# Kernel optimization log

Hardware: AMD Instinct MI355X
Metric: run time of the kernel (lower is better)

The kernel has to match this reference:

```python
import jax, jax.numpy as jnp
import numpy as np

B, S, H = 2, 2048, 1024
NUM_HEAD = 16
HEAD_HIDDEN = H // NUM_HEAD
SCALE = float(np.sqrt(HEAD_HIDDEN))  # 8.0
INF = 10000000000.0


def setup_inputs() -> dict:
    key = jax.random.key(0)
    ks = jax.random.split(key, 12)
    std = 1.0 / np.sqrt(H)
    mk = lambda k: (jax.random.normal(k, (H, H), jnp.float32) * std)
    return {
        "query": jax.random.normal(ks[0], (B, S, H), jnp.float32),
        "key": jax.random.normal(ks[1], (B, S, H), jnp.float32),
        "value": jax.random.normal(ks[2], (B, S, H), jnp.float32),
        "att_mask": jnp.ones((B, 1, 1, S), jnp.float32),
        "wq": mk(ks[3]), "bq": jnp.zeros((H,), jnp.float32),
        "wk": mk(ks[4]), "bk": jnp.zeros((H,), jnp.float32),
        "wv": mk(ks[5]), "bv": jnp.zeros((H,), jnp.float32),
        "wo": mk(ks[6]), "bo": jnp.zeros((H,), jnp.float32),
    }


def reference(query, key, value, att_mask, wq, bq, wk, bk, wv, bv, wo, bo):
    # projections (weights stored as [in, out])
    q = query @ wq + bq
    k = key @ wk + bk
    v = value @ wv + bv
    # split heads: [B, S, nH, hd]
    q = q.reshape(B, S, NUM_HEAD, HEAD_HIDDEN)
    k = k.reshape(B, S, NUM_HEAD, HEAD_HIDDEN)
    v = v.reshape(B, S, NUM_HEAD, HEAD_HIDDEN)
    # scores [B, nH, Sq, Sk], first divide by scale
    att = jnp.einsum("bqhd,bkhd->bhqk", q, k) / SCALE
    # additive mask applied BEFORE the second scale division (faithful quirk)
    att = att + (1.0 - att_mask) * (-INF)
    att = jax.nn.softmax(att / SCALE, axis=-1)
    out = jnp.einsum("bhqk,bkhd->bqhd", att, v).reshape(B, S, H)
    return out @ wo + bo
```

## Files before the change

kernel.cpp:

```cpp
#include <hip/hip_runtime.h>
#include <cstdint>

typedef unsigned short u16;
typedef __attribute__((ext_vector_type(8))) short bf16x8;
typedef __attribute__((ext_vector_type(4))) float f32x4;

#define S_LEN 2048
#define HDIM  1024
#define NHEAD 16

__device__ __forceinline__ float bf2f(u16 u){ return __uint_as_float(((uint32_t)u) << 16); }
__device__ __forceinline__ u16 f2bf(float f){
  uint32_t x = __float_as_uint(f);
  return (u16)((x + 0x7fffu + ((x >> 16) & 1u)) >> 16);
}

__device__ __forceinline__ void gload_lds16(const void* g, void* l){
  __builtin_amdgcn_global_load_lds((const __attribute__((address_space(1))) void*)g,
                                   (__attribute__((address_space(3))) void*)l, 16, 0, 0);
}

__global__ __launch_bounds__(256) void k_cvt3(const float* __restrict__ q, const float* __restrict__ k,
                                              const float* __restrict__ v, u16* __restrict__ oq,
                                              u16* __restrict__ ok, u16* __restrict__ ov){
  int z = blockIdx.y;
  const float* in = z == 0 ? q : (z == 1 ? k : v);
  u16* out = z == 0 ? oq : (z == 1 ? ok : ov);
  int i = blockIdx.x * 256 + threadIdx.x;
  float4 f0 = *(const float4*)&in[(size_t)i * 8];
  float4 f1 = *(const float4*)&in[(size_t)i * 8 + 4];
  bf16x8 o;
  o[0] = (short)f2bf(f0.x); o[1] = (short)f2bf(f0.y);
  o[2] = (short)f2bf(f0.z); o[3] = (short)f2bf(f0.w);
  o[4] = (short)f2bf(f1.x); o[5] = (short)f2bf(f1.y);
  o[6] = (short)f2bf(f1.z); o[7] = (short)f2bf(f1.w);
  *(bf16x8*)&out[(size_t)i * 8] = o;
}

__global__ __launch_bounds__(256) void k_tr_w4(const float* __restrict__ w0, const float* __restrict__ w1,
                                               const float* __restrict__ w2, const float* __restrict__ w3,
                                               u16* __restrict__ o0, u16* __restrict__ o1,
                                               u16* __restrict__ o2, u16* __restrict__ o3){
  int z = blockIdx.z;
  const float* in = z == 0 ? w0 : (z == 1 ? w1 : (z == 2 ? w2 : w3));
  u16* out = z == 0 ? o0 : (z == 1 ? o1 : (z == 2 ? o2 : o3));
  __shared__ float t[64][65];
  int r0 = threadIdx.x >> 6;
  int c  = threadIdx.x & 63;
  int bx = blockIdx.x * 64, by = blockIdx.y * 64;
  #pragma unroll
  for (int i = 0; i < 64; i += 4) t[r0 + i][c] = in[(size_t)(by + r0 + i) * 1024 + bx + c];
  __syncthreads();
  #pragma unroll
  for (int i = 0; i < 64; i += 4) out[(size_t)(bx + r0 + i) * 1024 + by + c] = f2bf(t[c][r0 + i]);
}

__global__ __launch_bounds__(256) void k_gemm_qkv(const u16* __restrict__ A0, const u16* __restrict__ A1,
                                                  const u16* __restrict__ A2,
                                                  const u16* __restrict__ W0, const u16* __restrict__ W1,
                                                  const u16* __restrict__ W2,
                                                  const float* __restrict__ b0, const float* __restrict__ b1,
                                                  const float* __restrict__ b2,
                                                  u16* __restrict__ C0, u16* __restrict__ C1,
                                                  u16* __restrict__ vt)
{
  int z = blockIdx.z;
  const u16* A  = z == 0 ? A0 : (z == 1 ? A1 : A2);
  const u16* Wt = z == 0 ? W0 : (z == 1 ? W1 : W2);
  const float* bias = z == 0 ? b0 : (z == 1 ? b1 : b2);

  __shared__ u16 As[128 * 32];
  __shared__ u16 Bs[128 * 32];
  const int K = 1024, N = 1024;
  int tid = threadIdx.x;
  int lane = tid & 63, wave = tid >> 6;
  int quad = lane >> 4, c16 = lane & 15;
  int wm = wave >> 1, wn = wave & 1;
  int m0 = blockIdx.x * 128, n0 = blockIdx.y * 128;

  f32x4 acc[4][4] = {};

  for (int k0 = 0; k0 < K; k0 += 32) {
    #pragma unroll
    for (int i = 0; i < 2; i++) {
      int slot = tid + i * 256;
      int r = slot >> 2, cc = (slot & 3) * 8;
      gload_lds16(&A [(size_t)(m0 + r) * K + k0 + cc], &As[slot * 8]);
      gload_lds16(&Wt[(size_t)(n0 + r) * K + k0 + cc], &Bs[slot * 8]);
    }
    __syncthreads();
    bf16x8 af[4], bfr[4];
    #pragma unroll
    for (int mt = 0; mt < 4; mt++) af[mt]  = *(const bf16x8*)&As[(wm * 64 + mt * 16 + c16) * 32 + quad * 8];
    #pragma unroll
    for (int nt = 0; nt < 4; nt++) bfr[nt] = *(const bf16x8*)&Bs[(wn * 64 + nt * 16 + c16) * 32 + quad * 8];
    #pragma unroll
    for (int mt = 0; mt < 4; mt++)
      #pragma unroll
      for (int nt = 0; nt < 4; nt++)
        acc[mt][nt] = __builtin_amdgcn_mfma_f32_16x16x32_bf16(af[mt], bfr[nt], acc[mt][nt], 0, 0, 0);
    __syncthreads();
  }

  if (z == 2) {
    #pragma unroll
    for (int nt = 0; nt < 4; nt++) {
      int gc = n0 + wn * 64 + nt * 16 + c16;
      int h = gc >> 6, d = gc & 63;
      float bv = bias[gc];
      #pragma unroll
      for (int mt = 0; mt < 4; mt++) {
        int gr0 = m0 + wm * 64 + mt * 16 + quad * 4;
        int bb = gr0 >> 11, s = gr0 & 2047;
        ushort4 pk;
        pk.x = f2bf(acc[mt][nt][0] + bv);
        pk.y = f2bf(acc[mt][nt][1] + bv);
        pk.z = f2bf(acc[mt][nt][2] + bv);
        pk.w = f2bf(acc[mt][nt][3] + bv);
        *(ushort4*)&vt[((size_t)(bb * NHEAD + h) * 64 + d) * S_LEN + s] = pk;
      }
    }
  } else {
    float scale = z == 0 ? (1.0f / 64.0f) : 1.0f;
    u16* C = z == 0 ? C0 : C1;
    #pragma unroll
    for (int nt = 0; nt < 4; nt++) {
      int gc = n0 + wn * 64 + nt * 16 + c16;
      float bv = bias[gc];
      #pragma unroll
      for (int mt = 0; mt < 4; mt++)
        #pragma unroll
        for (int r = 0; r < 4; r++) {
          int gr = m0 + wm * 64 + mt * 16 + quad * 4 + r;
          C[(size_t)gr * N + gc] = f2bf((acc[mt][nt][r] + bv) * scale);
        }
    }
  }
}

__global__ __launch_bounds__(256) void k_gemm_o(const u16* __restrict__ A, const u16* __restrict__ Wt,
                                                const float* __restrict__ bias, float* __restrict__ C)
{
  __shared__ u16 As[128 * 32];
  __shared__ u16 Bs[64 * 32];
  const int K = 1024, N = 1024;
  int tid = threadIdx.x;
  int lane = tid & 63, wave = tid >> 6;
  int quad = lane >> 4, c16 = lane & 15;
  int wm = wave >> 1, wn = wave & 1;
  int m0 = blockIdx.x * 128, n0 = blockIdx.y * 64;

  f32x4 acc[4][2] = {};

  for (int k0 = 0; k0 < K; k0 += 32) {
    #pragma unroll
    for (int i = 0; i < 2; i++) {
      int slot = tid + i * 256;
      int r = slot >> 2, cc = (slot & 3) * 8;
      gload_lds16(&A[(size_t)(m0 + r) * K + k0 + cc], &As[slot * 8]);
    }
    {
      int r = tid >> 2, cc = (tid & 3) * 8;
      gload_lds16(&Wt[(size_t)(n0 + r) * K + k0 + cc], &Bs[tid * 8]);
    }
    __syncthreads();
    bf16x8 af[4], bfr[2];
    #pragma unroll
    for (int mt = 0; mt < 4; mt++) af[mt]  = *(const bf16x8*)&As[(wm * 64 + mt * 16 + c16) * 32 + quad * 8];
    #pragma unroll
    for (int nt = 0; nt < 2; nt++) bfr[nt] = *(const bf16x8*)&Bs[(wn * 32 + nt * 16 + c16) * 32 + quad * 8];
    #pragma unroll
    for (int mt = 0; mt < 4; mt++)
      #pragma unroll
      for (int nt = 0; nt < 2; nt++)
        acc[mt][nt] = __builtin_amdgcn_mfma_f32_16x16x32_bf16(af[mt], bfr[nt], acc[mt][nt], 0, 0, 0);
    __syncthreads();
  }

  #pragma unroll
  for (int nt = 0; nt < 2; nt++) {
    int gc = n0 + wn * 32 + nt * 16 + c16;
    float bv = bias[gc];
    #pragma unroll
    for (int mt = 0; mt < 4; mt++)
      #pragma unroll
      for (int r = 0; r < 4; r++) {
        int gr = m0 + wm * 64 + mt * 16 + quad * 4 + r;
        C[(size_t)gr * N + gc] = acc[mt][nt][r] + bv;
      }
  }
}

__global__ __launch_bounds__(256, 2) void k_attn(const u16* __restrict__ Qm,
                                                 const u16* __restrict__ Km,
                                                 const u16* __restrict__ VTm,
                                                 const float* __restrict__ mask,
                                                 u16* __restrict__ Om)
{
  __shared__ u16 Ks[64][72];
  __shared__ u16 VTs[64][72];
  __shared__ u16 Ps[128][72];
  __shared__ float Ms[64];
  int tid = threadIdx.x;
  int lane = tid & 63, wave = tid >> 6;
  int quad = lane >> 4, c16 = lane & 15;
  int qb = blockIdx.x, h = blockIdx.y, b = blockIdx.z;
  const size_t SH = (size_t)S_LEN * HDIM;
  const u16* Qbase  = Qm + (size_t)b * SH + (size_t)qb * 128 * HDIM + h * 64;
  const u16* Kbase  = Km + (size_t)b * SH + h * 64;
  const u16* VTbase = VTm + (size_t)(b * NHEAD + h) * 64 * S_LEN;
  const float* Mbase = mask + (size_t)b * S_LEN;

  int qw0 = wave * 32;

  bf16x8 aq[2][2];
  #pragma unroll
  for (int mt = 0; mt < 2; mt++)
    #pragma unroll
    for (int kk = 0; kk < 2; kk++)
      aq[mt][kk] = *(const bf16x8*)&Qbase[(size_t)(qw0 + mt * 16 + c16) * HDIM + kk * 32 + quad * 8];

  f32x4 oacc[2][4] = {};
  float lsum[2][4] = {};

  for (int kt = 0; kt < S_LEN / 64; kt++) {
    int s0 = kt * 64;
    #pragma unroll
    for (int i = 0; i < 5; i++) {
      int c = i * 256 + tid;
      if (c < 576) {
        int r = c / 9, cc = c - r * 9;
        int col = (cc == 8) ? 0 : cc * 8;
        gload_lds16(&Kbase[(size_t)(s0 + r) * HDIM + col], &Ks[0][0] + c * 8);
      } else if (c < 1152) {
        int c2 = c - 576;
        int r = c2 / 9, cc = c2 - r * 9;
        int col = (cc == 8) ? 0 : cc * 8;
        gload_lds16(&VTbase[(size_t)r * S_LEN + s0 + col], &VTs[0][0] + c2 * 8);
      }
    }
    if (tid < 64) Ms[tid] = (1.0f - Mbase[s0 + tid]) * (-1.25e9f);
    __syncthreads();

    f32x4 sacc[2][4] = {};
    #pragma unroll
    for (int kk = 0; kk < 2; kk++) {
      bf16x8 bk[4];
      #pragma unroll
      for (int nt = 0; nt < 4; nt++) bk[nt] = *(const bf16x8*)&Ks[nt * 16 + c16][kk * 32 + quad * 8];
      #pragma unroll
      for (int mt = 0; mt < 2; mt++)
        #pragma unroll
        for (int nt = 0; nt < 4; nt++)
          sacc[mt][nt] = __builtin_amdgcn_mfma_f32_16x16x32_bf16(aq[mt][kk], bk[nt], sacc[mt][nt], 0, 0, 0);
    }

    #pragma unroll
    for (int nt = 0; nt < 4; nt++) {
      float madd = Ms[nt * 16 + c16];
      #pragma unroll
      for (int mt = 0; mt < 2; mt++)
        #pragma unroll
        for (int r = 0; r < 4; r++) {
          float p = __expf(sacc[mt][nt][r] + madd);
          lsum[mt][r] += p;
          Ps[qw0 + mt * 16 + quad * 4 + r][nt * 16 + c16] = f2bf(p);
        }
    }

    #pragma unroll
    for (int kk = 0; kk < 2; kk++) {
      bf16x8 pa[2], vb[4];
      #pragma unroll
      for (int mt = 0; mt < 2; mt++) pa[mt] = *(const bf16x8*)&Ps[qw0 + mt * 16 + c16][kk * 32 + quad * 8];
      #pragma unroll
      for (int nt = 0; nt < 4; nt++) vb[nt] = *(const bf16x8*)&VTs[nt * 16 + c16][kk * 32 + quad * 8];
      #pragma unroll
      for (int mt = 0; mt < 2; mt++)
        #pragma unroll
        for (int nt = 0; nt < 4; nt++)
          oacc[mt][nt] = __builtin_amdgcn_mfma_f32_16x16x32_bf16(pa[mt], vb[nt], oacc[mt][nt], 0, 0, 0);
    }
    __syncthreads();
  }

  #pragma unroll
  for (int mt = 0; mt < 2; mt++)
    #pragma unroll
    for (int r = 0; r < 4; r++) {
      float v = lsum[mt][r];
      v += __shfl_xor(v, 1); v += __shfl_xor(v, 2); v += __shfl_xor(v, 4); v += __shfl_xor(v, 8);
      lsum[mt][r] = v;
    }

  u16* Obase = Om + (size_t)b * SH + (size_t)qb * 128 * HDIM + h * 64;
  #pragma unroll
  for (int mt = 0; mt < 2; mt++)
    #pragma unroll
    for (int nt = 0; nt < 4; nt++)
      #pragma unroll
      for (int r = 0; r < 4; r++) {
        int lr = qw0 + mt * 16 + quad * 4 + r;
        Obase[(size_t)lr * HDIM + nt * 16 + c16] = f2bf(oacc[mt][nt][r] / lsum[mt][r]);
      }
}

extern "C" void kernel_launch(void* const* d_in, const int* in_sizes, int n_in,
                              void* d_out, int out_size, void* d_ws, size_t ws_size,
                              hipStream_t stream)
{
  (void)in_sizes; (void)n_in; (void)out_size; (void)ws_size;
  const float* q_in = (const float*)d_in[0];
  const float* k_in = (const float*)d_in[1];
  const float* v_in = (const float*)d_in[2];
  const float* mask = (const float*)d_in[3];
  const float* wq   = (const float*)d_in[4];
  const float* bq   = (const float*)d_in[5];
  const float* wk   = (const float*)d_in[6];
  const float* bk   = (const float*)d_in[7];
  const float* wv   = (const float*)d_in[8];
  const float* bv   = (const float*)d_in[9];
  const float* wo   = (const float*)d_in[10];
  const float* bo   = (const float*)d_in[11];

  u16* ws  = (u16*)d_ws;
  u16* wqt = ws;
  u16* wkt = wqt + (1u << 20);
  u16* wvt = wkt + (1u << 20);
  u16* wot = wvt + (1u << 20);
  u16* qi_ = wot + (1u << 20);
  u16* ki_ = qi_ + (4u << 20);
  u16* vi_ = ki_ + (4u << 20);
  u16* qb_ = vi_ + (4u << 20);
  u16* kb_ = qb_ + (4u << 20);
  u16* vtb = kb_ + (4u << 20);
  u16* ob_ = vtb + (4u << 20);

  dim3 blk(256);
  k_cvt3<<<dim3(2048, 3), blk, 0, stream>>>(q_in, k_in, v_in, qi_, ki_, vi_);
  k_tr_w4<<<dim3(16, 16, 4), blk, 0, stream>>>(wq, wk, wv, wo, wqt, wkt, wvt, wot);
  k_gemm_qkv<<<dim3(32, 8, 3), blk, 0, stream>>>(qi_, ki_, vi_, wqt, wkt, wvt, bq, bk, bv, qb_, kb_, vtb);
  k_attn<<<dim3(16, 16, 2), blk, 0, stream>>>(qb_, kb_, vtb, mask, ob_);
  k_gemm_o<<<dim3(32, 16), blk, 0, stream>>>(ob_, wot, bo, (float*)d_out);
}
```

Baseline: 252.3 us.

## Load K/V tiles directly into registers in attention and add separate V transpose

```diff
diff --git a/kernel.cpp b/kernel.cpp
--- a/kernel.cpp
+++ b/kernel.cpp
@@ -55,6 +55,21 @@
   for (int i = 0; i < 64; i += 4) out[(size_t)(bx + r0 + i) * 1024 + by + c] = f2bf(t[c][r0 + i]);
 }
 
+__global__ __launch_bounds__(256) void k_tr_v(const u16* __restrict__ v, u16* __restrict__ vt){
+  __shared__ u16 t[64][65];
+  int r0 = threadIdx.x >> 6, c = threadIdx.x & 63;
+  int s0 = blockIdx.x * 64;
+  int bh = blockIdx.y;
+  int b = bh >> 4, h = bh & 15;
+  const u16* src = v + (size_t)b * S_LEN * HDIM + h * 64;
+  #pragma unroll
+  for (int i = 0; i < 64; i += 4) t[r0 + i][c] = src[(size_t)(s0 + r0 + i) * HDIM + c];
+  __syncthreads();
+  u16* dst = vt + (size_t)bh * 64 * S_LEN + s0;
+  #pragma unroll
+  for (int i = 0; i < 64; i += 4) dst[(size_t)(r0 + i) * S_LEN + c] = t[c][r0 + i];
+}
+
 __global__ __launch_bounds__(256) void k_gemm_qkv(const u16* __restrict__ A0, const u16* __restrict__ A1,
                                                   const u16* __restrict__ A2,
                                                   const u16* __restrict__ W0, const u16* __restrict__ W1,
@@ -62,12 +77,14 @@
                                                   const float* __restrict__ b0, const float* __restrict__ b1,
                                                   const float* __restrict__ b2,
                                                   u16* __restrict__ C0, u16* __restrict__ C1,
-                                                  u16* __restrict__ vt)
+                                                  u16* __restrict__ C2)
 {
   int z = blockIdx.z;
   const u16* A  = z == 0 ? A0 : (z == 1 ? A1 : A2);
   const u16* Wt = z == 0 ? W0 : (z == 1 ? W1 : W2);
   const float* bias = z == 0 ? b0 : (z == 1 ? b1 : b2);
+  u16* C = z == 0 ? C0 : (z == 1 ? C1 : C2);
+  float scale = z == 0 ? (1.0f / 64.0f) : 1.0f;
 
   __shared__ u16 As[128 * 32];
   __shared__ u16 Bs[128 * 32];
@@ -102,39 +119,17 @@
     __syncthreads();
   }
 
-  if (z == 2) {
-    #pragma unroll
-    for (int nt = 0; nt < 4; nt++) {
-      int gc = n0 + wn * 64 + nt * 16 + c16;
-      int h = gc >> 6, d = gc & 63;
-      float bv = bias[gc];
-      #pragma unroll
-      for (int mt = 0; mt < 4; mt++) {
-        int gr0 = m0 + wm * 64 + mt * 16 + quad * 4;
-        int bb = gr0 >> 11, s = gr0 & 2047;
-        ushort4 pk;
-        pk.x = f2bf(acc[mt][nt][0] + bv);
-        pk.y = f2bf(acc[mt][nt][1] + bv);
-        pk.z = f2bf(acc[mt][nt][2] + bv);
-        pk.w = f2bf(acc[mt][nt][3] + bv);
-        *(ushort4*)&vt[((size_t)(bb * NHEAD + h) * 64 + d) * S_LEN + s] = pk;
+  #pragma unroll
+  for (int nt = 0; nt < 4; nt++) {
+    int gc = n0 + wn * 64 + nt * 16 + c16;
+    float bv = bias[gc];
+    #pragma unroll
+    for (int mt = 0; mt < 4; mt++)
+      #pragma unroll
+      for (int r = 0; r < 4; r++) {
+        int gr = m0 + wm * 64 + mt * 16 + quad * 4 + r;
+        C[(size_t)gr * N + gc] = f2bf((acc[mt][nt][r] + bv) * scale);
       }
-    }
-  } else {
-    float scale = z == 0 ? (1.0f / 64.0f) : 1.0f;
-    u16* C = z == 0 ? C0 : C1;
-    #pragma unroll
-    for (int nt = 0; nt < 4; nt++) {
-      int gc = n0 + wn * 64 + nt * 16 + c16;
-      float bv = bias[gc];
-      #pragma unroll
-      for (int mt = 0; mt < 4; mt++)
-        #pragma unroll
-        for (int r = 0; r < 4; r++) {
-          int gr = m0 + wm * 64 + mt * 16 + quad * 4 + r;
-          C[(size_t)gr * N + gc] = f2bf((acc[mt][nt][r] + bv) * scale);
-        }
-    }
   }
 }
 
@@ -197,10 +192,8 @@
                                                  const float* __restrict__ mask,
                                                  u16* __restrict__ Om)
 {
-  __shared__ u16 Ks[64][72];
-  __shared__ u16 VTs[64][72];
   __shared__ u16 Ps[128][72];
-  __shared__ float Ms[64];
+  __shared__ float Msall[S_LEN];
   int tid = threadIdx.x;
   int lane = tid & 63, wave = tid >> 6;
   int quad = lane >> 4, c16 = lane & 15;
@@ -211,6 +204,8 @@
   const u16* VTbase = VTm + (size_t)(b * NHEAD + h) * 64 * S_LEN;
   const float* Mbase = mask + (size_t)b * S_LEN;
 
+  for (int i = tid; i < S_LEN; i += 256) Msall[i] = (1.0f - Mbase[i]) * (-1.25e9f);
+
   int qw0 = wave * 32;
 
   bf16x8 aq[2][2];
@@ -223,41 +218,45 @@
   f32x4 oacc[2][4] = {};
   float lsum[2][4] = {};
 
-  for (int kt = 0; kt < S_LEN / 64; kt++) {
+  bf16x8 bkA[2][4], bkB[2][4];
+  #pragma unroll
+  for (int kk = 0; kk < 2; kk++)
+    #pragma unroll
+    for (int nt = 0; nt < 4; nt++)
+      bkA[kk][nt] = *(const bf16x8*)&Kbase[(size_t)(nt * 16 + c16) * HDIM + kk * 32 + quad * 8];
+
+  __syncthreads();
+
+  auto body = [&](int kt, bf16x8 (&cur)[2][4], bf16x8 (&nxt)[2][4]) {
     int s0 = kt * 64;
-    #pragma unroll
-    for (int i = 0; i < 5; i++) {
-      int c = i * 256 + tid;
-      if (c < 576) {
-        int r = c / 9, cc = c - r * 9;
-        int col = (cc == 8) ? 0 : cc * 8;
-        gload_lds16(&Kbase[(size_t)(s0 + r) * HDIM + col], &Ks[0][0] + c * 8);
-      } else if (c < 1152) {
-        int c2 = c - 576;
-        int r = c2 / 9, cc = c2 - r * 9;
-        int col = (cc == 8) ? 0 : cc * 8;
-        gload_lds16(&VTbase[(size_t)r * S_LEN + s0 + col], &VTs[0][0] + c2 * 8);
-      }
-    }
-    if (tid < 64) Ms[tid] = (1.0f - Mbase[s0 + tid]) * (-1.25e9f);
-    __syncthreads();
+    bf16x8 vb[2][4];
+    #pragma unroll
+    for (int kk = 0; kk < 2; kk++)
+      #pragma unroll
+      for (int nt = 0; nt < 4; nt++)
+        vb[kk][nt] = *(const bf16x8*)&VTbase[(size_t)(nt * 16 + c16) * S_LEN + s0 + kk * 32 + quad * 8];
 
     f32x4 sacc[2][4] = {};
     #pragma unroll
-    for (int kk = 0; kk < 2; kk++) {
-      bf16x8 bk[4];
-      #pragma unroll
-      for (int nt = 0; nt < 4; nt++) bk[nt] = *(const bf16x8*)&Ks[nt * 16 + c16][kk * 32 + quad * 8];
+    for (int kk = 0; kk < 2; kk++)
       #pragma unroll
       for (int mt = 0; mt < 2; mt++)
         #pragma unroll
         for (int nt = 0; nt < 4; nt++)
-          sacc[mt][nt] = __builtin_amdgcn_mfma_f32_16x16x32_bf16(aq[mt][kk], bk[nt], sacc[mt][nt], 0, 0, 0);
+          sacc[mt][nt] = __builtin_amdgcn_mfma_f32_16x16x32_bf16(aq[mt][kk], cur[kk][nt], sacc[mt][nt], 0, 0, 0);
+
+    if (kt + 1 < S_LEN / 64) {
+      int s1 = s0 + 64;
+      #pragma unroll
+      for (int kk = 0; kk < 2; kk++)
+        #pragma unroll
+        for (int nt = 0; nt < 4; nt++)
+          nxt[kk][nt] = *(const bf16x8*)&Kbase[(size_t)(s1 + nt * 16 + c16) * HDIM + kk * 32 + quad * 8];
     }
 
     #pragma unroll
     for (int nt = 0; nt < 4; nt++) {
-      float madd = Ms[nt * 16 + c16];
+      float madd = Msall[s0 + nt * 16 + c16];
       #pragma unroll
       for (int mt = 0; mt < 2; mt++)
         #pragma unroll
@@ -270,18 +269,20 @@
 
     #pragma unroll
     for (int kk = 0; kk < 2; kk++) {
-      bf16x8 pa[2], vb[4];
+      bf16x8 pa[2];
       #pragma unroll
       for (int mt = 0; mt < 2; mt++) pa[mt] = *(const bf16x8*)&Ps[qw0 + mt * 16 + c16][kk * 32 + quad * 8];
-      #pragma unroll
-      for (int nt = 0; nt < 4; nt++) vb[nt] = *(const bf16x8*)&VTs[nt * 16 + c16][kk * 32 + quad * 8];
       #pragma unroll
       for (int mt = 0; mt < 2; mt++)
         #pragma unroll
         for (int nt = 0; nt < 4; nt++)
-          oacc[mt][nt] = __builtin_amdgcn_mfma_f32_16x16x32_bf16(pa[mt], vb[nt], oacc[mt][nt], 0, 0, 0);
-    }
-    __syncthreads();
+          oacc[mt][nt] = __builtin_amdgcn_mfma_f32_16x16x32_bf16(pa[mt], vb[kk][nt], oacc[mt][nt], 0, 0, 0);
+    }
+  };
+
+  for (int kt = 0; kt < S_LEN / 64; kt += 2) {
+    body(kt,     bkA, bkB);
+    body(kt + 1, bkB, bkA);
   }
 
   #pragma unroll
@@ -333,13 +334,15 @@
   u16* vi_ = ki_ + (4u << 20);
   u16* qb_ = vi_ + (4u << 20);
   u16* kb_ = qb_ + (4u << 20);
-  u16* vtb = kb_ + (4u << 20);
+  u16* vb_ = kb_ + (4u << 20);
+  u16* vtb = vb_ + (4u << 20);
   u16* ob_ = vtb + (4u << 20);
 
   dim3 blk(256);
   k_cvt3<<<dim3(2048, 3), blk, 0, stream>>>(q_in, k_in, v_in, qi_, ki_, vi_);
   k_tr_w4<<<dim3(16, 16, 4), blk, 0, stream>>>(wq, wk, wv, wo, wqt, wkt, wvt, wot);
-  k_gemm_qkv<<<dim3(32, 8, 3), blk, 0, stream>>>(qi_, ki_, vi_, wqt, wkt, wvt, bq, bk, bv, qb_, kb_, vtb);
+  k_gemm_qkv<<<dim3(32, 8, 3), blk, 0, stream>>>(qi_, ki_, vi_, wqt, wkt, wvt, bq, bk, bv, qb_, kb_, vb_);
+  k_tr_v<<<dim3(32, 32), blk, 0, stream>>>(vb_, vtb);
   k_attn<<<dim3(16, 16, 2), blk, 0, stream>>>(qb_, kb_, vtb, mask, ob_);
   k_gemm_o<<<dim3(32, 16), blk, 0, stream>>>(ob_, wot, bo, (float*)d_out);
 }
```

Result: slower. 298.3 us (+18.2%).
